# Kernel tuning notes

Measured on AMD Instinct MI355X. Metric: run time of the kernel, lower is better.

The kernel has to match this reference:

```python
import jax, jax.numpy as jnp
import numpy as np

D_MODEL = 256
N_HEAD = 4
HEAD_DIM = D_MODEL // N_HEAD  # 64


def setup_inputs() -> dict:
    key = jax.random.key(0)
    kx, kw, kb = jax.random.split(key, 3)
    x = jax.random.normal(kx, (4, 2048, D_MODEL), dtype=jnp.float32)
    # nn.Linear(256, 768): weight [768, 256], bias [768]
    bound = 1.0 / np.sqrt(D_MODEL)
    W_qkv = jax.random.uniform(kw, (3 * D_MODEL, D_MODEL), dtype=jnp.float32, minval=-bound, maxval=bound)
    b_qkv = jax.random.uniform(kb, (3 * D_MODEL,), dtype=jnp.float32, minval=-bound, maxval=bound)
    return {"x": x, "W_qkv": W_qkv, "b_qkv": b_qkv}


def reference(x, W_qkv, b_qkv):
    B, S, _ = x.shape
    # fused QKV projection: [B, S, 3*D]
    qkv = jnp.einsum("bsd,ed->bse", x, W_qkv) + b_qkv
    q, k, v = jnp.split(qkv, 3, axis=-1)
    # [B, S, D] -> [B, H, S, Dh]
    def to_heads(t):
        return t.reshape(B, S, N_HEAD, HEAD_DIM).transpose(0, 2, 1, 3)
    q, k, v = to_heads(q), to_heads(k), to_heads(v)
    scale = 1.0 / np.sqrt(HEAD_DIM)
    # scores [B, H, S, S]
    scores = jnp.einsum("bhqd,bhkd->bhqk", q, k) * scale
    attn = jax.nn.softmax(scores, axis=-1)
    out = jnp.einsum("bhqk,bhkd->bhqd", attn, v)  # [B, H, S, Dh]
    return out
```

## Files before the change

### kernel.cpp

```cpp
#include <hip/hip_runtime.h>

#define BB 4
#define SS 2048
#define DM 256
#define NH 4
#define DH 64
#define NROW (BB*SS)
#define NE   (3*DM)
#define BH   (BB*NH)
#define HEAD_ELEMS (BH*SS*DH)
#define NQROWS (BH*SS)

typedef _Float16 half_t;
typedef __attribute__((ext_vector_type(8))) _Float16 half8;
typedef __attribute__((ext_vector_type(4))) _Float16 half4;
typedef __attribute__((ext_vector_type(4))) float floatx4;

#define KPAD 72

__global__ __launch_bounds__(256) void prep(const float* __restrict__ x,
                                            const float* __restrict__ W,
                                            half_t* __restrict__ xh,
                                            half_t* __restrict__ xl,
                                            half_t* __restrict__ wh) {
    int gtid = blockIdx.x * 256 + threadIdx.x;
    {
        int i = gtid * 4;
        float4 v = *(const float4*)&x[i];
        half4 h, l;
        h.x = (half_t)v.x; l.x = (half_t)(v.x - (float)h.x);
        h.y = (half_t)v.y; l.y = (half_t)(v.y - (float)h.y);
        h.z = (half_t)v.z; l.z = (half_t)(v.z - (float)h.z);
        h.w = (half_t)v.w; l.w = (half_t)(v.w - (float)h.w);
        *(half4*)&xh[i] = h;
        *(half4*)&xl[i] = l;
    }
    if (gtid < NE * DM / 4) {
        int i = gtid * 4;
        float4 v = *(const float4*)&W[i];
        half4 h;
        h.x = (half_t)v.x; h.y = (half_t)v.y;
        h.z = (half_t)v.z; h.w = (half_t)v.w;
        *(half4*)&wh[i] = h;
    }
}

__global__ __launch_bounds__(256) void qkv_proj(const half_t* __restrict__ xh,
                                                const half_t* __restrict__ xl,
                                                const half_t* __restrict__ whg,
                                                const float* __restrict__ bias,
                                                half_t* __restrict__ qh,
                                                half_t* __restrict__ kh,
                                                half_t* __restrict__ vt) {
    __shared__ __align__(16) half_t Xh[64 * KPAD];
    __shared__ __align__(16) half_t Xl[64 * KPAD];
    __shared__ __align__(16) half_t Wh[64 * KPAD];

    const int rb   = blockIdx.x * 64;
    const int nb   = blockIdx.y * 64;
    const int tid  = threadIdx.x;
    const int wid  = tid >> 6;
    const int lane = tid & 63;
    const int quad = lane >> 4;
    const int col  = lane & 15;

    floatx4 acc[4];
    #pragma unroll
    for (int t = 0; t < 4; ++t) acc[t] = (floatx4){0.f, 0.f, 0.f, 0.f};

    for (int k0 = 0; k0 < DM; k0 += 64) {
        __syncthreads();
        #pragma unroll
        for (int i = 0; i < 2; ++i) {
            int gi = tid + 256 * i;
            int r  = gi >> 3;
            int c8 = (gi & 7) * 8;
            *(half8*)&Xh[r * KPAD + c8] = *(const half8*)&xh[(size_t)(rb + r) * DM + k0 + c8];
            *(half8*)&Xl[r * KPAD + c8] = *(const half8*)&xl[(size_t)(rb + r) * DM + k0 + c8];
            *(half8*)&Wh[r * KPAD + c8] = *(const half8*)&whg[(size_t)(nb + r) * DM + k0 + c8];
        }
        __syncthreads();

        half8 ah0 = *(const half8*)&Xh[(wid * 16 + col) * KPAD + quad * 8];
        half8 ah1 = *(const half8*)&Xh[(wid * 16 + col) * KPAD + 32 + quad * 8];
        half8 al0 = *(const half8*)&Xl[(wid * 16 + col) * KPAD + quad * 8];
        half8 al1 = *(const half8*)&Xl[(wid * 16 + col) * KPAD + 32 + quad * 8];

        #pragma unroll
        for (int t = 0; t < 4; ++t) {
            half8 bh0 = *(const half8*)&Wh[(t * 16 + col) * KPAD + quad * 8];
            half8 bh1 = *(const half8*)&Wh[(t * 16 + col) * KPAD + 32 + quad * 8];
            acc[t] = __builtin_amdgcn_mfma_f32_16x16x32_f16(ah0, bh0, acc[t], 0, 0, 0);
            acc[t] = __builtin_amdgcn_mfma_f32_16x16x32_f16(ah1, bh1, acc[t], 0, 0, 0);
            acc[t] = __builtin_amdgcn_mfma_f32_16x16x32_f16(al0, bh0, acc[t], 0, 0, 0);
            acc[t] = __builtin_amdgcn_mfma_f32_16x16x32_f16(al1, bh1, acc[t], 0, 0, 0);
        }
    }

    const int part = nb >> 8;
    const int mloc = wid * 16 + quad * 4;
    if (part != 2) {
        #pragma unroll
        for (int t = 0; t < 4; ++t) {
            int e    = nb + t * 16 + col;
            float be = bias[e];
            int dm   = e & 255;
            int h    = dm >> 6;
            int dh   = dm & 63;
            #pragma unroll
            for (int r = 0; r < 4; ++r) {
                int row = rb + mloc + r;
                int b   = row >> 11;
                int s   = row & 2047;
                int bh_ = b * NH + h;
                float val = acc[t][r] + be;
                if (part == 0) {
                    qh[((size_t)bh_ * SS + s) * DH + dh] = (half_t)(val * 0.125f);
                } else {
                    kh[((size_t)bh_ * SS + s) * DH + dh] = (half_t)val;
                }
            }
        }
    } else {
        __syncthreads();
        #pragma unroll
        for (int t = 0; t < 4; ++t) {
            int e    = nb + t * 16 + col;
            float be = bias[e];
            #pragma unroll
            for (int r = 0; r < 4; ++r)
                Xh[(t * 16 + col) * KPAD + mloc + r] = (half_t)(acc[t][r] + be);
        }
        __syncthreads();
        const int b   = rb >> 11;
        const int s0  = rb & 2047;
        const int h   = (nb >> 6) & 3;
        const int bh_ = b * NH + h;
        #pragma unroll
        for (int i = 0; i < 2; ++i) {
            int idx = tid + 256 * i;
            int rr  = idx >> 3;
            int cc8 = (idx & 7) * 8;
            *(half8*)&vt[((size_t)bh_ * DH + rr) * SS + s0 + cc8] =
                *(const half8*)&Xh[rr * KPAD + cc8];
        }
    }
}

__global__ __launch_bounds__(128) void attn(const half_t* __restrict__ qh,
                                            const half_t* __restrict__ kh,
                                            const half_t* __restrict__ vt,
                                            half_t* __restrict__ pO,
                                            float* __restrict__ mst,
                                            float* __restrict__ lst) {
    __shared__ __align__(16) half_t Ks[64 * KPAD];
    __shared__ __align__(16) half_t Vts[64 * KPAD];

    const int q0   = blockIdx.x * 64;
    const int bh   = blockIdx.y;
    const int kz   = blockIdx.z;
    const size_t base = (size_t)bh * SS * DH;
    const int tid  = threadIdx.x;
    const int wid  = tid >> 6;
    const int lane = tid & 63;
    const int quad = lane >> 4;
    const int col  = lane & 15;
    const int ktBeg = kz * (SS / 2);
    const int ktEnd = ktBeg + (SS / 2);

    int srr[4], scc[4];
    #pragma unroll
    for (int i = 0; i < 4; ++i) {
        int gi = tid + 128 * i;
        srr[i] = gi >> 3;
        scc[i] = (gi & 7) * 8;
    }

    half8 bq[2][2];
    #pragma unroll
    for (int st = 0; st < 2; ++st) {
        int s = q0 + wid * 32 + st * 16 + col;
        bq[st][0] = *(const half8*)&qh[base + (size_t)s * DH + quad * 8];
        bq[st][1] = *(const half8*)&qh[base + (size_t)s * DH + 32 + quad * 8];
    }

    half8 ck[4], cv[4], nk[4], nv[4];
    #pragma unroll
    for (int i = 0; i < 4; ++i) {
        ck[i] = *(const half8*)&kh[base + (size_t)(ktBeg + srr[i]) * DH + scc[i]];
        cv[i] = *(const half8*)&vt[base + (size_t)srr[i] * SS + ktBeg + scc[i]];
        nk[i] = ck[i];
        nv[i] = cv[i];
    }

    float m_i[2] = {-3.0e38f, -3.0e38f};
    float l_i[2] = {0.f, 0.f};
    floatx4 o[2][4];
    #pragma unroll
    for (int st = 0; st < 2; ++st)
        #pragma unroll
        for (int dt = 0; dt < 4; ++dt) o[st][dt] = (floatx4){0.f, 0.f, 0.f, 0.f};

    for (int kt = ktBeg; kt < ktEnd; kt += 64) {
        __syncthreads();
        #pragma unroll
        for (int i = 0; i < 4; ++i) {
            *(half8*)&Ks[srr[i] * KPAD + scc[i]]  = ck[i];
            *(half8*)&Vts[srr[i] * KPAD + scc[i]] = cv[i];
        }
        __syncthreads();

        const int ktn = kt + 64;
        if (ktn < ktEnd) {
            #pragma unroll
            for (int i = 0; i < 4; ++i) {
                nk[i] = *(const half8*)&kh[base + (size_t)(ktn + srr[i]) * DH + scc[i]];
                nv[i] = *(const half8*)&vt[base + (size_t)srr[i] * SS + ktn + scc[i]];
            }
        }

        floatx4 sc[2][4];
        #pragma unroll
        for (int t = 0; t < 4; ++t) {
            half8 ak0 = *(const half8*)&Ks[(t * 16 + col) * KPAD + quad * 8];
            half8 ak1 = *(const half8*)&Ks[(t * 16 + col) * KPAD + 32 + quad * 8];
            #pragma unroll
            for (int st = 0; st < 2; ++st) {
                floatx4 c = (floatx4){0.f, 0.f, 0.f, 0.f};
                c = __builtin_amdgcn_mfma_f32_16x16x32_f16(ak0, bq[st][0], c, 0, 0, 0);
                c = __builtin_amdgcn_mfma_f32_16x16x32_f16(ak1, bq[st][1], c, 0, 0, 0);
                sc[st][t] = c;
            }
        }

        half4 pa[2][4];
        #pragma unroll
        for (int st = 0; st < 2; ++st) {
            float mloc = -3.0e38f;
            #pragma unroll
            for (int t = 0; t < 4; ++t)
                #pragma unroll
                for (int r = 0; r < 4; ++r)
                    mloc = fmaxf(mloc, sc[st][t][r]);
            mloc = fmaxf(mloc, __shfl_xor(mloc, 16));
            mloc = fmaxf(mloc, __shfl_xor(mloc, 32));
            float m_new = fmaxf(m_i[st], mloc);
            float alpha = __expf(m_i[st] - m_new);
            m_i[st] = m_new;

            float rsum = 0.f;
            #pragma unroll
            for (int t = 0; t < 4; ++t) {
                float p0 = __expf(sc[st][t][0] - m_new);
                float p1 = __expf(sc[st][t][1] - m_new);
                float p2 = __expf(sc[st][t][2] - m_new);
                float p3 = __expf(sc[st][t][3] - m_new);
                rsum += p0 + p1 + p2 + p3;
                pa[st][t] = (half4){(half_t)p0, (half_t)p1, (half_t)p2, (half_t)p3};
            }
            rsum += __shfl_xor(rsum, 16);
            rsum += __shfl_xor(rsum, 32);
            l_i[st] = l_i[st] * alpha + rsum;

            float ar[4];
            #pragma unroll
            for (int i = 0; i < 4; ++i) ar[i] = __shfl(alpha, quad * 4 + i);
            #pragma unroll
            for (int dt = 0; dt < 4; ++dt)
                #pragma unroll
                for (int i = 0; i < 4; ++i)
                    o[st][dt][i] *= ar[i];
        }

        #pragma unroll
        for (int t = 0; t < 4; ++t) {
            #pragma unroll
            for (int dt = 0; dt < 4; ++dt) {
                half4 bv = *(const half4*)&Vts[(dt * 16 + col) * KPAD + t * 16 + quad * 4];
                #pragma unroll
                for (int st = 0; st < 2; ++st)
                    o[st][dt] = __builtin_amdgcn_mfma_f32_16x16x16f16(pa[st][t], bv, o[st][dt], 0, 0, 0);
            }
        }

        #pragma unroll
        for (int i = 0; i < 4; ++i) { ck[i] = nk[i]; cv[i] = nv[i]; }
    }

    const size_t pbase = (size_t)kz * HEAD_ELEMS + base;
    #pragma unroll
    for (int st = 0; st < 2; ++st) {
        float inv = 1.0f / l_i[st];
        float ir[4];
        #pragma unroll
        for (int i = 0; i < 4; ++i) ir[i] = __shfl(inv, quad * 4 + i);
        #pragma unroll
        for (int dt = 0; dt < 4; ++dt)
            #pragma unroll
            for (int i = 0; i < 4; ++i) {
                int row = q0 + wid * 32 + st * 16 + quad * 4 + i;
                pO[pbase + (size_t)row * DH + dt * 16 + col] = (half_t)(o[st][dt][i] * ir[i]);
            }
        if (quad == 0) {
            int row = q0 + wid * 32 + st * 16 + col;
            int idx = kz * NQROWS + bh * SS + row;
            mst[idx] = m_i[st];
            lst[idx] = l_i[st];
        }
    }
}

__global__ __launch_bounds__(256) void merge(const half_t* __restrict__ pO,
                                             const float* __restrict__ mst,
                                             const float* __restrict__ lst,
                                             float* __restrict__ out) {
    int gid = blockIdx.x * 256 + threadIdx.x;
    int row = gid >> 3;
    int dc  = (gid & 7) * 8;
    float m1 = mst[row], m2 = mst[NQROWS + row];
    float l1 = lst[row], l2 = lst[NQROWS + row];
    float M  = fmaxf(m1, m2);
    float w1 = l1 * __expf(m1 - M);
    float w2 = l2 * __expf(m2 - M);
    float inv = 1.0f / (w1 + w2);
    float a = w1 * inv, b = w2 * inv;
    half8 o1 = *(const half8*)&pO[(size_t)row * DH + dc];
    half8 o2 = *(const half8*)&pO[(size_t)HEAD_ELEMS + (size_t)row * DH + dc];
    float4 r0, r1;
    r0.x = a * (float)o1[0] + b * (float)o2[0];
    r0.y = a * (float)o1[1] + b * (float)o2[1];
    r0.z = a * (float)o1[2] + b * (float)o2[2];
    r0.w = a * (float)o1[3] + b * (float)o2[3];
    r1.x = a * (float)o1[4] + b * (float)o2[4];
    r1.y = a * (float)o1[5] + b * (float)o2[5];
    r1.z = a * (float)o1[6] + b * (float)o2[6];
    r1.w = a * (float)o1[7] + b * (float)o2[7];
    *(float4*)&out[(size_t)row * DH + dc]     = r0;
    *(float4*)&out[(size_t)row * DH + dc + 4] = r1;
}

extern "C" void kernel_launch(void* const* d_in, const int* in_sizes, int n_in,
                              void* d_out, int out_size, void* d_ws, size_t ws_size,
                              hipStream_t stream) {
    const float* x  = (const float*)d_in[0];
    const float* Wq = (const float*)d_in[1];
    const float* bq = (const float*)d_in[2];
    float* out = (float*)d_out;

    half_t* qh  = (half_t*)d_ws;
    half_t* kh  = qh + (size_t)HEAD_ELEMS;
    half_t* vt  = kh + (size_t)HEAD_ELEMS;
    half_t* xh  = vt + (size_t)HEAD_ELEMS;
    half_t* xl  = xh + (size_t)HEAD_ELEMS;
    half_t* whp = xl + (size_t)HEAD_ELEMS;
    half_t* pO  = xh;
    float*  mst = (float*)((char*)d_ws + 21364736);
    float*  lst = mst + 2 * NQROWS;

    prep<<<2048, 256, 0, stream>>>(x, Wq, xh, xl, whp);
    qkv_proj<<<dim3(NROW / 64, NE / 64), 256, 0, stream>>>(xh, xl, whp, bq, qh, kh, vt);
    attn<<<dim3(SS / 64, BH, 2), 128, 0, stream>>>(qh, kh, vt, pO, mst, lst);
    merge<<<1024, 256, 0, stream>>>(pO, mst, lst, out);
}
```

Baseline: 120.6 us.

## Double-buffer K/V in LDS, lazy softmax rescale, exp2 and MFMA row sums

The attention kernel now double-buffers the K and V tiles in shared memory, so each iteration needs one barrier instead of two and the next tile's store overlaps with compute. The log2(e) factor is folded into the Q scale so the softmax can use exp2f. The running max is updated lazily: rescaling of the accumulator happens only when some lane's max actually grows. Row sums are computed by an extra MFMA against a ones vector instead of shuffles. Final normalization moves to the merge kernel, which lowers per-block epilogue work at the cost of more LDS, an extra MFMA per tile, and storing unnormalized partial outputs in fp16.

```diff
diff --git a/kernel.cpp b/kernel.cpp
--- a/kernel.cpp
+++ b/kernel.cpp
@@ -17,6 +17,7 @@
 typedef __attribute__((ext_vector_type(4))) float floatx4;
 
 #define KPAD 72
+#define QSCALE 0.1803368801111120f
 
 __global__ __launch_bounds__(256) void prep(const float* __restrict__ x,
                                             const float* __restrict__ W,
@@ -115,7 +116,7 @@
                 int bh_ = b * NH + h;
                 float val = acc[t][r] + be;
                 if (part == 0) {
-                    qh[((size_t)bh_ * SS + s) * DH + dh] = (half_t)(val * 0.125f);
+                    qh[((size_t)bh_ * SS + s) * DH + dh] = (half_t)(val * QSCALE);
                 } else {
                     kh[((size_t)bh_ * SS + s) * DH + dh] = (half_t)val;
                 }
@@ -147,14 +148,14 @@
     }
 }
 
-__global__ __launch_bounds__(128) void attn(const half_t* __restrict__ qh,
-                                            const half_t* __restrict__ kh,
-                                            const half_t* __restrict__ vt,
-                                            half_t* __restrict__ pO,
-                                            float* __restrict__ mst,
-                                            float* __restrict__ lst) {
-    __shared__ __align__(16) half_t Ks[64 * KPAD];
-    __shared__ __align__(16) half_t Vts[64 * KPAD];
+__global__ __launch_bounds__(128, 2) void attn(const half_t* __restrict__ qh,
+                                               const half_t* __restrict__ kh,
+                                               const half_t* __restrict__ vt,
+                                               half_t* __restrict__ pO,
+                                               float* __restrict__ mst,
+                                               float* __restrict__ lst) {
+    __shared__ __align__(16) half_t Ks[2][64 * KPAD];
+    __shared__ __align__(16) half_t Vts[2][64 * KPAD];
 
     const int q0   = blockIdx.x * 64;
     const int bh   = blockIdx.y;
@@ -167,6 +168,7 @@
     const int col  = lane & 15;
     const int ktBeg = kz * (SS / 2);
     const int ktEnd = ktBeg + (SS / 2);
+    const int NIT   = (SS / 2) / 64;
 
     int srr[4], scc[4];
     #pragma unroll
@@ -184,46 +186,63 @@
         bq[st][1] = *(const half8*)&qh[base + (size_t)s * DH + 32 + quad * 8];
     }
 
-    half8 ck[4], cv[4], nk[4], nv[4];
+    half8 ck[4], cv[4];
     #pragma unroll
     for (int i = 0; i < 4; ++i) {
         ck[i] = *(const half8*)&kh[base + (size_t)(ktBeg + srr[i]) * DH + scc[i]];
         cv[i] = *(const half8*)&vt[base + (size_t)srr[i] * SS + ktBeg + scc[i]];
-        nk[i] = ck[i];
-        nv[i] = cv[i];
-    }
-
-    float m_i[2] = {-3.0e38f, -3.0e38f};
-    float l_i[2] = {0.f, 0.f};
+    }
+    #pragma unroll
+    for (int i = 0; i < 4; ++i) {
+        *(half8*)&Ks[0][srr[i] * KPAD + scc[i]]  = ck[i];
+        *(half8*)&Vts[0][srr[i] * KPAD + scc[i]] = cv[i];
+    }
+    __syncthreads();
+    {
+        const int kt1 = (ktBeg + 64 < ktEnd) ? ktBeg + 64 : ktBeg;
+        #pragma unroll
+        for (int i = 0; i < 4; ++i) {
+            ck[i] = *(const half8*)&kh[base + (size_t)(kt1 + srr[i]) * DH + scc[i]];
+            cv[i] = *(const half8*)&vt[base + (size_t)srr[i] * SS + kt1 + scc[i]];
+        }
+    }
+
+    const half4 bone = (half4){(half_t)1.f, (half_t)1.f, (half_t)1.f, (half_t)1.f};
+    float m_i[2] = {0.f, 0.f};
+    floatx4 lacc[2];
     floatx4 o[2][4];
     #pragma unroll
-    for (int st = 0; st < 2; ++st)
+    for (int st = 0; st < 2; ++st) {
+        lacc[st] = (floatx4){0.f, 0.f, 0.f, 0.f};
         #pragma unroll
         for (int dt = 0; dt < 4; ++dt) o[st][dt] = (floatx4){0.f, 0.f, 0.f, 0.f};
-
-    for (int kt = ktBeg; kt < ktEnd; kt += 64) {
-        __syncthreads();
+    }
+
+    for (int it = 0; it < NIT; ++it) {
+        const int buf = it & 1;
+        const int kt  = ktBeg + it * 64;
+
         #pragma unroll
         for (int i = 0; i < 4; ++i) {
-            *(half8*)&Ks[srr[i] * KPAD + scc[i]]  = ck[i];
-            *(half8*)&Vts[srr[i] * KPAD + scc[i]] = cv[i];
-        }
-        __syncthreads();
-
-        const int ktn = kt + 64;
-        if (ktn < ktEnd) {
+            *(half8*)&Ks[buf ^ 1][srr[i] * KPAD + scc[i]]  = ck[i];
+            *(half8*)&Vts[buf ^ 1][srr[i] * KPAD + scc[i]] = cv[i];
+        }
+
+        {
+            int kt2 = kt + 128;
+            if (kt2 >= ktEnd) kt2 = ktBeg;
             #pragma unroll
             for (int i = 0; i < 4; ++i) {
-                nk[i] = *(const half8*)&kh[base + (size_t)(ktn + srr[i]) * DH + scc[i]];
-                nv[i] = *(const half8*)&vt[base + (size_t)srr[i] * SS + ktn + scc[i]];
+                ck[i] = *(const half8*)&kh[base + (size_t)(kt2 + srr[i]) * DH + scc[i]];
+                cv[i] = *(const half8*)&vt[base + (size_t)srr[i] * SS + kt2 + scc[i]];
             }
         }
 
         floatx4 sc[2][4];
         #pragma unroll
         for (int t = 0; t < 4; ++t) {
-            half8 ak0 = *(const half8*)&Ks[(t * 16 + col) * KPAD + quad * 8];
-            half8 ak1 = *(const half8*)&Ks[(t * 16 + col) * KPAD + 32 + quad * 8];
+            half8 ak0 = *(const half8*)&Ks[buf][(t * 16 + col) * KPAD + quad * 8];
+            half8 ak1 = *(const half8*)&Ks[buf][(t * 16 + col) * KPAD + 32 + quad * 8];
             #pragma unroll
             for (int st = 0; st < 2; ++st) {
                 floatx4 c = (floatx4){0.f, 0.f, 0.f, 0.f};
@@ -236,76 +255,89 @@
         half4 pa[2][4];
         #pragma unroll
         for (int st = 0; st < 2; ++st) {
-            float mloc = -3.0e38f;
+            float mloc = fmaxf(fmaxf(fmaxf(sc[st][0][0], sc[st][0][1]), fmaxf(sc[st][0][2], sc[st][0][3])),
+                               fmaxf(fmaxf(sc[st][1][0], sc[st][1][1]), fmaxf(sc[st][1][2], sc[st][1][3])));
+            mloc = fmaxf(mloc,
+                   fmaxf(fmaxf(fmaxf(sc[st][2][0], sc[st][2][1]), fmaxf(sc[st][2][2], sc[st][2][3])),
+                         fmaxf(fmaxf(sc[st][3][0], sc[st][3][1]), fmaxf(sc[st][3][2], sc[st][3][3]))));
+            float mx = fmaxf(mloc, __shfl_xor(mloc, 16));
+            mx = fmaxf(mx, __shfl_xor(mx, 32));
+
+            float p[16];
+            if (it == 0) {
+                m_i[st] = mx;
+                #pragma unroll
+                for (int t = 0; t < 4; ++t)
+                    #pragma unroll
+                    for (int r = 0; r < 4; ++r)
+                        p[t * 4 + r] = exp2f(sc[st][t][r] - mx);
+            } else {
+                #pragma unroll
+                for (int t = 0; t < 4; ++t)
+                    #pragma unroll
+                    for (int r = 0; r < 4; ++r)
+                        p[t * 4 + r] = exp2f(sc[st][t][r] - m_i[st]);
+                if (__any(mx > m_i[st])) {
+                    float m_new = fmaxf(m_i[st], mx);
+                    float beta  = exp2f(m_i[st] - m_new);
+                    m_i[st] = m_new;
+                    #pragma unroll
+                    for (int j = 0; j < 16; ++j) p[j] *= beta;
+                    float ar[4];
+                    #pragma unroll
+                    for (int i = 0; i < 4; ++i) ar[i] = __shfl(beta, quad * 4 + i);
+                    #pragma unroll
+                    for (int dt = 0; dt < 4; ++dt)
+                        #pragma unroll
+                        for (int i = 0; i < 4; ++i)
+                            o[st][dt][i] *= ar[i];
+                    #pragma unroll
+                    for (int i = 0; i < 4; ++i) lacc[st][i] *= ar[i];
+                }
+            }
             #pragma unroll
             for (int t = 0; t < 4; ++t)
-                #pragma unroll
-                for (int r = 0; r < 4; ++r)
-                    mloc = fmaxf(mloc, sc[st][t][r]);
-            mloc = fmaxf(mloc, __shfl_xor(mloc, 16));
-            mloc = fmaxf(mloc, __shfl_xor(mloc, 32));
-            float m_new = fmaxf(m_i[st], mloc);
-            float alpha = __expf(m_i[st] - m_new);
-            m_i[st] = m_new;
-
-            float rsum = 0.f;
-            #pragma unroll
-            for (int t = 0; t < 4; ++t) {
-                float p0 = __expf(sc[st][t][0] - m_new);
-                float p1 = __expf(sc[st][t][1] - m_new);
-                float p2 = __expf(sc[st][t][2] - m_new);
-                float p3 = __expf(sc[st][t][3] - m_new);
-                rsum += p0 + p1 + p2 + p3;
-                pa[st][t] = (half4){(half_t)p0, (half_t)p1, (half_t)p2, (half_t)p3};
-            }
-            rsum += __shfl_xor(rsum, 16);
-            rsum += __shfl_xor(rsum, 32);
-            l_i[st] = l_i[st] * alpha + rsum;
-
-            float ar[4];
-            #pragma unroll
-            for (int i = 0; i < 4; ++i) ar[i] = __shfl(alpha, quad * 4 + i);
-            #pragma unroll
-            for (int dt = 0; dt < 4; ++dt)
-                #pragma unroll
-                for (int i = 0; i < 4; ++i)
-                    o[st][dt][i] *= ar[i];
+                pa[st][t] = (half4){(half_t)p[t * 4 + 0], (half_t)p[t * 4 + 1],
+                                    (half_t)p[t * 4 + 2], (half_t)p[t * 4 + 3]};
         }
 
         #pragma unroll
         for (int t = 0; t < 4; ++t) {
             #pragma unroll
             for (int dt = 0; dt < 4; ++dt) {
-                half4 bv = *(const half4*)&Vts[(dt * 16 + col) * KPAD + t * 16 + quad * 4];
+                half4 bv = *(const half4*)&Vts[buf][(dt * 16 + col) * KPAD + t * 16 + quad * 4];
                 #pragma unroll
                 for (int st = 0; st < 2; ++st)
                     o[st][dt] = __builtin_amdgcn_mfma_f32_16x16x16f16(pa[st][t], bv, o[st][dt], 0, 0, 0);
             }
-        }
-
-        #pragma unroll
-        for (int i = 0; i < 4; ++i) { ck[i] = nk[i]; cv[i] = nv[i]; }
+            #pragma unroll
+            for (int st = 0; st < 2; ++st)
+                lacc[st] = __builtin_amdgcn_mfma_f32_16x16x16f16(pa[st][t], bone, lacc[st], 0, 0, 0);
+        }
+
+        __syncthreads();
     }
 
     const size_t pbase = (size_t)kz * HEAD_ELEMS + base;
     #pragma unroll
     for (int st = 0; st < 2; ++st) {
-        float inv = 1.0f / l_i[st];
-        float ir[4];
-        #pragma unroll
-        for (int i = 0; i < 4; ++i) ir[i] = __shfl(inv, quad * 4 + i);
         #pragma unroll
         for (int dt = 0; dt < 4; ++dt)
             #pragma unroll
             for (int i = 0; i < 4; ++i) {
                 int row = q0 + wid * 32 + st * 16 + quad * 4 + i;
-                pO[pbase + (size_t)row * DH + dt * 16 + col] = (half_t)(o[st][dt][i] * ir[i]);
+                pO[pbase + (size_t)row * DH + dt * 16 + col] = (half_t)o[st][dt][i];
             }
         if (quad == 0) {
             int row = q0 + wid * 32 + st * 16 + col;
-            int idx = kz * NQROWS + bh * SS + row;
-            mst[idx] = m_i[st];
-            lst[idx] = l_i[st];
+            mst[kz * NQROWS + bh * SS + row] = m_i[st];
+        }
+        if (col == 0) {
+            #pragma unroll
+            for (int r = 0; r < 4; ++r) {
+                int row = q0 + wid * 32 + st * 16 + quad * 4 + r;
+                lst[kz * NQROWS + bh * SS + row] = lacc[st][r];
+            }
         }
     }
 }
@@ -320,10 +352,10 @@
     float m1 = mst[row], m2 = mst[NQROWS + row];
     float l1 = lst[row], l2 = lst[NQROWS + row];
     float M  = fmaxf(m1, m2);
-    float w1 = l1 * __expf(m1 - M);
-    float w2 = l2 * __expf(m2 - M);
-    float inv = 1.0f / (w1 + w2);
-    float a = w1 * inv, b = w2 * inv;
+    float e1 = exp2f(m1 - M);
+    float e2 = exp2f(m2 - M);
+    float inv = 1.0f / (l1 * e1 + l2 * e2);
+    float a = e1 * inv, b = e2 * inv;
     half8 o1 = *(const half8*)&pO[(size_t)row * DH + dc];
     half8 o2 = *(const half8*)&pO[(size_t)HEAD_ELEMS + (size_t)row * DH + dc];
     float4 r0, r1;
```

Result: slower. 126.1 us (+4.6%).
